# Performance work log

Measured on AMD Instinct MI355X. Metric: run time of the kernel, lower is better.

## Reference

```python
import jax, jax.numpy as jnp
import numpy as np

DIM = 1024
NHEADS = 16
DIM_HEAD = 64
HIDDEN = NHEADS * DIM_HEAD  # 1024


def _xavier(key, fan_in, fan_out):
    limit = np.sqrt(6.0 / (fan_in + fan_out))
    return jax.random.uniform(key, (fan_in, fan_out), jnp.float32, -limit, limit)


def setup_inputs() -> dict:
    key = jax.random.key(0)
    kq, k1, k2, k3 = jax.random.split(key, 4)
    q = jax.random.normal(kq, (2, 2048, DIM), jnp.float32)
    Wq = _xavier(k1, DIM, HIDDEN)
    bq = jnp.zeros((HIDDEN,), jnp.float32)
    Wkv = _xavier(k2, DIM, 2 * HIDDEN)
    bkv = jnp.zeros((2 * HIDDEN,), jnp.float32)
    Wo = _xavier(k3, HIDDEN, DIM)
    bo = jnp.zeros((DIM,), jnp.float32)
    return {"q": q, "Wq": Wq, "bq": bq, "Wkv": Wkv, "bkv": bkv, "Wo": Wo, "bo": bo}


def reference(q, Wq, bq, Wkv, bkv, Wo, bo):
    scale = DIM_HEAD ** (-0.5)
    query = q @ Wq + bq                      # [b, s, hidden]
    kv = q @ Wkv + bkv                       # self-attention: kv from q
    key_, value = jnp.split(kv, 2, axis=-1)  # [b, s, hidden] each
    b, s, _ = query.shape
    query = query.reshape(b, s, NHEADS, DIM_HEAD)
    key_ = key_.reshape(b, s, NHEADS, DIM_HEAD)
    value = value.reshape(b, s, NHEADS, DIM_HEAD)
    scores = jnp.einsum('bqhd,bkhd->bhqk', query, key_) * scale
    attn = jax.nn.softmax(scores, axis=-1)
    out = jnp.einsum('bhqk,bkhd->bqhd', attn, value)
    out = out.reshape(b, s, HIDDEN)
    return out @ Wo + bo
```

## Files before the change

kernel.cpp:

```cpp
#include <hip/hip_runtime.h>

#define DIM 1024
#define NHEADS 16
#define DH 64
#define BATCH 2
#define SEQ 2048

typedef float f32x4 __attribute__((ext_vector_type(4)));
typedef short s16x8 __attribute__((ext_vector_type(8)));
typedef short s16x4 __attribute__((ext_vector_type(4)));

__device__ __forceinline__ short f2bf(float f) {
    union { float f; unsigned u; } v; v.f = f;
    unsigned r = v.u + 0x7fffu + ((v.u >> 16) & 1u);
    return (short)(r >> 16);
}

#if defined(__has_builtin)
#if __has_builtin(__builtin_amdgcn_cvt_pk_bf16_f32)
#define HAVE_PK_BF16 1
#endif
#endif
__device__ __forceinline__ unsigned f2bf_pk(float a, float b) {
#ifdef HAVE_PK_BF16
    typedef __bf16 bf16x2_t __attribute__((ext_vector_type(2)));
    bf16x2_t r = __builtin_amdgcn_cvt_pk_bf16_f32(a, b);
    return __builtin_bit_cast(unsigned, r);
#else
    return ((unsigned)(unsigned short)f2bf(b) << 16) | (unsigned short)f2bf(a);
#endif
}
__device__ __forceinline__ s16x4 pk4(float a, float b, float c, float d) {
    union { unsigned u[2]; s16x4 v; } x;
    x.u[0] = f2bf_pk(a, b); x.u[1] = f2bf_pk(c, d);
    return x.v;
}

#if defined(__has_builtin)
#if __has_builtin(__builtin_amdgcn_exp2f)
#define EXP2(x) __builtin_amdgcn_exp2f(x)
#endif
#endif
#ifndef EXP2
#define EXP2(x) exp2f(x)
#endif

__device__ __forceinline__ void gld16(const void* g, void* l) {
    __builtin_amdgcn_global_load_lds(
        (const __attribute__((address_space(1))) void*)g,
        (__attribute__((address_space(3))) void*)l, 16, 0, 0);
}

__global__ __launch_bounds__(256) void convert_bf16_kernel(
    const float* __restrict__ X, short* __restrict__ Y)
{
    const int i = (blockIdx.x * 256 + threadIdx.x) * 8;
    float4 a = *(const float4*)(X + i);
    float4 b = *(const float4*)(X + i + 4);
    union { unsigned u[4]; s16x8 v; } o;
    o.u[0] = f2bf_pk(a.x, a.y); o.u[1] = f2bf_pk(a.z, a.w);
    o.u[2] = f2bf_pk(b.x, b.y); o.u[3] = f2bf_pk(b.z, b.w);
    *(s16x8*)(Y + i) = o.v;
}

__global__ __launch_bounds__(256) void transpose_w_kernel(
    const float* __restrict__ Wq, const float* __restrict__ Wkv,
    const float* __restrict__ Wo, short* __restrict__ WT)
{
    const int t  = threadIdx.x;
    const int ng = blockIdx.x * 64 + (t & 63);
    const int k0 = (blockIdx.y * 4 + (t >> 6)) * 8;
    const float* W; int n, N;
    if (ng < 1024)      { W = Wq;  n = ng;        N = 1024; }
    else if (ng < 3072) { W = Wkv; n = ng - 1024; N = 2048; }
    else                { W = Wo;  n = ng - 3072; N = 1024; }
    float v[8];
#pragma unroll
    for (int j = 0; j < 8; ++j) v[j] = W[(size_t)(k0 + j) * N + n];
    union { unsigned u[4]; s16x8 s; } o;
    o.u[0] = f2bf_pk(v[0], v[1]); o.u[1] = f2bf_pk(v[2], v[3]);
    o.u[2] = f2bf_pk(v[4], v[5]); o.u[3] = f2bf_pk(v[6], v[7]);
    *(s16x8*)&WT[(size_t)ng * 1024 + k0] = o.s;
}

__global__ __launch_bounds__(256) void transpose_v_kernel(
    const short* __restrict__ QKV, short* __restrict__ VtG)
{
    const int t = threadIdx.x;
    const int tok0 = blockIdx.x * 64;
    const int h = blockIdx.y, b = blockIdx.z;
    __shared__ short L[64 * 72];
    const short* src = QKV + (size_t)(b * SEQ + tok0) * 3072 + 2048 + h * 64;
#pragma unroll
    for (int p = 0; p < 2; ++p) {
        int r = p * 32 + (t >> 3);
        *(s16x8*)&L[r * 72 + (t & 7) * 8] = *(const s16x8*)(src + (size_t)r * 3072 + (t & 7) * 8);
    }
    __syncthreads();
    short* dst = VtG + (size_t)(b * NHEADS + h) * 64 * SEQ + tok0;
#pragma unroll
    for (int p = 0; p < 2; ++p) {
        int u = p * 256 + t;
        int dv = u >> 3, c = (u & 7) * 8;
        s16x8 o;
#pragma unroll
        for (int j = 0; j < 8; ++j) o[j] = L[(c + j) * 72 + dv];
        *(s16x8*)(dst + (size_t)dv * SEQ + c) = o;
    }
}

template<int TM, bool OUT_BF16>
__global__ __launch_bounds__(256) void gemm_mfma_kernel(
    const short* __restrict__ A, const short* __restrict__ Bt,
    const float* __restrict__ bias0, const float* __restrict__ bias1, int nsplit,
    float s0, float s1, void* __restrict__ C, int M, int N)
{
    const int K = 1024;
    constexpr int NI = (TM == 128) ? 4 : 2;
    __shared__ short As[TM * 32];
    __shared__ short Bs[128 * 32];

    const int t    = threadIdx.x;
    const int wave = t >> 6;
    const int lane = t & 63;
    const int col  = lane & 15;
    const int quad = lane >> 4;
    const int m0 = blockIdx.y * TM;
    const int n0 = blockIdx.x * 128;
    const int wroff = (TM == 128) ? (wave >> 1) * 64 : 0;
    const int wcoff = (TM == 128) ? (wave & 1) * 64 : wave * 32;

    f32x4 acc[4][NI];
#pragma unroll
    for (int mi = 0; mi < 4; ++mi)
#pragma unroll
        for (int ni = 0; ni < NI; ++ni) acc[mi][ni] = (f32x4){0.f, 0.f, 0.f, 0.f};

    constexpr int RPW = TM / 4;
    const int ldrowA = wave * RPW + (lane >> 2);
    const int ldrowB = wave * 32  + (lane >> 2);
    const int ldcol  = (lane & 3) * 8;
    const short* Ag = A  + (size_t)(m0 + ldrowA) * K + ldcol;
    const short* Bg = Bt + (size_t)(n0 + ldrowB) * K + ldcol;
    short* AsW = &As[wave * RPW * 32];
    short* BsW = &Bs[wave * 1024];

    for (int k0 = 0; k0 < K; k0 += 32) {
        __syncthreads();
        gld16(Ag + k0, AsW);
        if (TM == 128) gld16(Ag + 16 * K + k0, AsW + 512);
        gld16(Bg + k0,          BsW);
        gld16(Bg + 16 * K + k0, BsW + 512);
        __syncthreads();

        s16x8 aA[4], bB[NI];
#pragma unroll
        for (int mi = 0; mi < 4; ++mi)
            aA[mi] = *(const s16x8*)&As[(wroff + 16 * mi + col) * 32 + quad * 8];
#pragma unroll
        for (int ni = 0; ni < NI; ++ni)
            bB[ni] = *(const s16x8*)&Bs[(wcoff + 16 * ni + col) * 32 + quad * 8];
#pragma unroll
        for (int mi = 0; mi < 4; ++mi)
#pragma unroll
            for (int ni = 0; ni < NI; ++ni)
                acc[mi][ni] = __builtin_amdgcn_mfma_f32_16x16x32_bf16(aA[mi], bB[ni], acc[mi][ni], 0, 0, 0);
    }

    float bias_v[NI], scale_v[NI];
#pragma unroll
    for (int ni = 0; ni < NI; ++ni) {
        int nb = n0 + wcoff + 16 * ni + col;
        bias_v[ni]  = (nb < nsplit) ? bias0[nb] : bias1[nb - nsplit];
        scale_v[ni] = (nb < nsplit) ? s0 : s1;
    }

#pragma unroll
    for (int mi = 0; mi < 4; ++mi)
#pragma unroll
        for (int ni = 0; ni < NI; ++ni)
#pragma unroll
            for (int r = 0; r < 4; ++r) {
                const int gm = m0 + wroff + 16 * mi + quad * 4 + r;
                const int gn = n0 + wcoff + 16 * ni + col;
                float v = (acc[mi][ni][r] + bias_v[ni]) * scale_v[ni];
                if (OUT_BF16) ((short*)C)[(size_t)gm * N + gn] = f2bf(v);
                else          ((float*)C)[(size_t)gm * N + gn] = v;
            }
}

__global__ __launch_bounds__(512) void attn_v6_kernel(
    const short* __restrict__ QKV,
    const short* __restrict__ VtG,
    short* __restrict__ O)
{
    const int qt = blockIdx.x;
    const int h  = blockIdx.y;
    const int b  = blockIdx.z;
    const int t  = threadIdx.x;
    const int wave = t >> 6;
    const int lane = t & 63;
    const int col  = lane & 15;
    const int quad = lane >> 4;
    const int wq = wave & 3;
    const int kh = wave >> 2;

    __shared__ short Ks[2][64 * 72];
    __shared__ short Vt[2][64 * 72];
    __shared__ short Ps[8][64 * 40];

    const short* Qg = QKV + (size_t)(b * SEQ + qt * 256) * 3072 + h * DH;
    const short* Kg = QKV + (size_t)(b * SEQ) * 3072 + 1024 + h * DH;
    const short* VtRow = VtG + (size_t)(b * NHEADS + h) * 64 * SEQ;

    s16x8 aQ[4][2];
#pragma unroll
    for (int tq = 0; tq < 4; ++tq)
#pragma unroll
        for (int kq = 0; kq < 2; ++kq)
            aQ[tq][kq] = *(const s16x8*)(Qg + (size_t)(wq * 64 + 16 * tq + col) * 3072 + kq * 32 + quad * 8);

    f32x4 oa[4][4];
    float lsum[4] = {0.f, 0.f, 0.f, 0.f};
#pragma unroll
    for (int td = 0; td < 4; ++td)
#pragma unroll
        for (int tq = 0; tq < 4; ++tq) oa[td][tq] = (f32x4){0.f, 0.f, 0.f, 0.f};

    const int srow = t >> 3;
    const int sc8  = (t & 7) * 8;
    const short* KgS  = Kg + (size_t)srow * 3072 + sc8;
    const short* VtgS = VtRow + (size_t)srow * SEQ + sc8;
    s16x8 kx = *(const s16x8*)KgS;
    s16x8 vx = *(const s16x8*)VtgS;

    short* PsW = &Ps[wave][0];

    for (int kt = 0; kt < SEQ / 64; ++kt) {
        const int cur = kt & 1;
        *(s16x8*)&Ks[cur][srow * 72 + sc8] = kx;
        *(s16x8*)&Vt[cur][srow * 72 + sc8] = vx;
        {
            int nt = (kt + 1 < SEQ / 64) ? kt + 1 : kt;
            kx = *(const s16x8*)(KgS + (size_t)nt * 64 * 3072);
            vx = *(const s16x8*)(VtgS + (size_t)nt * 64);
        }
        __syncthreads();

        s16x8 aK[2][2];
#pragma unroll
        for (int tk = 0; tk < 2; ++tk)
#pragma unroll
            for (int kq = 0; kq < 2; ++kq)
                aK[tk][kq] = *(const s16x8*)&Ks[cur][(kh * 32 + 16 * tk + col) * 72 + kq * 32 + quad * 8];
        f32x4 st[2][4];
#pragma unroll
        for (int tk = 0; tk < 2; ++tk)
#pragma unroll
            for (int tq = 0; tq < 4; ++tq) {
                f32x4 a = (f32x4){0.f, 0.f, 0.f, 0.f};
                a = __builtin_amdgcn_mfma_f32_16x16x32_bf16(aK[tk][0], aQ[tq][0], a, 0, 0, 0);
                a = __builtin_amdgcn_mfma_f32_16x16x32_bf16(aK[tk][1], aQ[tq][1], a, 0, 0, 0);
                st[tk][tq] = a;
            }

#pragma unroll
        for (int tk = 0; tk < 2; ++tk)
#pragma unroll
            for (int tq = 0; tq < 4; ++tq) {
                float p0 = EXP2(st[tk][tq][0]);
                float p1 = EXP2(st[tk][tq][1]);
                float p2 = EXP2(st[tk][tq][2]);
                float p3 = EXP2(st[tk][tq][3]);
                lsum[tq] += (p0 + p1) + (p2 + p3);
                *(s16x4*)&PsW[(16 * tq + col) * 40 + 16 * tk + quad * 4] = pk4(p0, p1, p2, p3);
            }
        asm volatile("s_waitcnt lgkmcnt(0)" ::: "memory");

        s16x8 bP[4];
#pragma unroll
        for (int tq = 0; tq < 4; ++tq)
            bP[tq] = *(const s16x8*)&PsW[(16 * tq + col) * 40 + quad * 8];
#pragma unroll
        for (int td = 0; td < 4; ++td) {
            const int dv = 16 * td + col;
            s16x8 aV = *(const s16x8*)&Vt[cur][dv * 72 + kh * 32 + quad * 8];
#pragma unroll
            for (int tq = 0; tq < 4; ++tq)
                oa[td][tq] = __builtin_amdgcn_mfma_f32_16x16x32_bf16(aV, bP[tq], oa[td][tq], 0, 0, 0);
        }
    }

#pragma unroll
    for (int tq = 0; tq < 4; ++tq) {
        lsum[tq] += __shfl_xor(lsum[tq], 16);
        lsum[tq] += __shfl_xor(lsum[tq], 32);
    }

    __syncthreads();
    float* red  = (float*)&Ps[0][0];
    float* redl = red + 8192;
#pragma unroll
    for (int round = 0; round < 2; ++round) {
        if (wave >= 4 && ((wave >> 1) & 1) == round) {
            const int slot = wave & 1;
#pragma unroll
            for (int td = 0; td < 4; ++td)
#pragma unroll
                for (int tq = 0; tq < 4; ++tq)
#pragma unroll
                    for (int r = 0; r < 4; ++r)
                        red[slot * 4096 + (16 * td + quad * 4 + r) * 64 + 16 * tq + col] = oa[td][tq][r];
            if (quad == 0)
#pragma unroll
                for (int tq = 0; tq < 4; ++tq)
                    redl[slot * 64 + 16 * tq + col] = lsum[tq];
        }
        __syncthreads();
        if (wave < 4 && ((wave >> 1) & 1) == round) {
            const int slot = wave & 1;
#pragma unroll
            for (int td = 0; td < 4; ++td)
#pragma unroll
                for (int tq = 0; tq < 4; ++tq)
#pragma unroll
                    for (int r = 0; r < 4; ++r)
                        oa[td][tq][r] += red[slot * 4096 + (16 * td + quad * 4 + r) * 64 + 16 * tq + col];
#pragma unroll
            for (int tq = 0; tq < 4; ++tq)
                lsum[tq] += redl[slot * 64 + 16 * tq + col];
        }
        __syncthreads();
    }

    if (wave < 4) {
        short* Og = O + (size_t)(b * SEQ + qt * 256 + wq * 64) * DIM + h * DH;
        float inv[4];
#pragma unroll
        for (int tq = 0; tq < 4; ++tq) inv[tq] = 1.f / lsum[tq];
#pragma unroll
        for (int td = 0; td < 4; ++td)
#pragma unroll
            for (int tq = 0; tq < 4; ++tq)
                *(s16x4*)(Og + (size_t)(16 * tq + col) * DIM + 16 * td + quad * 4) =
                    pk4(oa[td][tq][0] * inv[tq], oa[td][tq][1] * inv[tq],
                        oa[td][tq][2] * inv[tq], oa[td][tq][3] * inv[tq]);
    }
}

extern "C" void kernel_launch(void* const* d_in, const int* in_sizes, int n_in,
                              void* d_out, int out_size, void* d_ws, size_t ws_size,
                              hipStream_t stream)
{
    const float* q   = (const float*)d_in[0];
    const float* Wq  = (const float*)d_in[1];
    const float* bq  = (const float*)d_in[2];
    const float* Wkv = (const float*)d_in[3];
    const float* bkv = (const float*)d_in[4];
    const float* Wo  = (const float*)d_in[5];
    const float* bo  = (const float*)d_in[6];
    float* out = (float*)d_out;

    const int M = BATCH * SEQ;

    short* qb     = (short*)d_ws;
    short* WT     = qb     + (size_t)M * DIM;
    short* QKVbuf = WT     + (size_t)4096 * DIM;
    short* AObuf  = QKVbuf + (size_t)M * 3 * DIM;
    short* VtG    = (short*)d_out;

    const float QSCALE = 0.18033688011112042f;

    convert_bf16_kernel<<<(M * DIM) / (256 * 8), 256, 0, stream>>>(q, qb);
    transpose_w_kernel<<<dim3(64, 32), 256, 0, stream>>>(Wq, Wkv, Wo, WT);

    gemm_mfma_kernel<128, true><<<dim3(3 * DIM / 128, M / 128), 256, 0, stream>>>(
        qb, WT, bq, bkv, DIM, QSCALE, 1.0f, QKVbuf, M, 3 * DIM);
    transpose_v_kernel<<<dim3(SEQ / 64, NHEADS, BATCH), 256, 0, stream>>>(QKVbuf, VtG);
    attn_v6_kernel<<<dim3(SEQ / 256, NHEADS, BATCH), 512, 0, stream>>>(QKVbuf, VtG, AObuf);
    gemm_mfma_kernel<64, false><<<dim3(DIM / 128, M / 64), 256, 0, stream>>>(
        AObuf, WT + (size_t)3072 * 1024, bo, bo, 1 << 30, 1.0f, 1.0f, out, M, DIM);
}
```

Baseline: 199.7 us.

## Keep P in registers via 16x16x16 MFMA, fuse V transpose into QKV GEMM

The attention kernel now feeds exp'd scores straight from accumulator registers as the B operand of 16x16x16 bf16 MFMAs. This drops the per-wave LDS round trip for P and its waitcnt, and shrinks shared memory, which may raise occupancy. The QKV GEMM epilogue writes the V columns already transposed into VtG, so the separate transpose_v kernel is gone. The convert and weight-transpose kernels are merged into one launch. The cost is twice as many MFMA instructions for PV at half the K depth, plus strided 8-byte stores in the GEMM epilogue.

```diff
diff --git a/kernel.cpp b/kernel.cpp
--- a/kernel.cpp
+++ b/kernel.cpp
@@ -45,67 +45,59 @@
 #define EXP2(x) exp2f(x)
 #endif
 
+#if defined(__has_builtin)
+#if __has_builtin(__builtin_amdgcn_mfma_f32_16x16x16bf16_1k)
+#define MFMA16(a, b, c) __builtin_amdgcn_mfma_f32_16x16x16bf16_1k(a, b, c, 0, 0, 0)
+#elif __has_builtin(__builtin_amdgcn_mfma_f32_16x16x16_bf16)
+#define MFMA16(a, b, c) __builtin_amdgcn_mfma_f32_16x16x16_bf16(a, b, c, 0, 0, 0)
+#endif
+#endif
+#ifndef MFMA16
+__device__ __forceinline__ f32x4 mfma16_asm(s16x4 a, s16x4 b, f32x4 c) {
+    f32x4 d;
+    asm volatile("v_mfma_f32_16x16x16_bf16 %0, %1, %2, %3"
+                 : "=v"(d) : "v"(a), "v"(b), "0"(c));
+    return d;
+}
+#define MFMA16(a, b, c) mfma16_asm(a, b, c)
+#endif
+
 __device__ __forceinline__ void gld16(const void* g, void* l) {
     __builtin_amdgcn_global_load_lds(
         (const __attribute__((address_space(1))) void*)g,
         (__attribute__((address_space(3))) void*)l, 16, 0, 0);
 }
 
-__global__ __launch_bounds__(256) void convert_bf16_kernel(
-    const float* __restrict__ X, short* __restrict__ Y)
-{
-    const int i = (blockIdx.x * 256 + threadIdx.x) * 8;
-    float4 a = *(const float4*)(X + i);
-    float4 b = *(const float4*)(X + i + 4);
-    union { unsigned u[4]; s16x8 v; } o;
-    o.u[0] = f2bf_pk(a.x, a.y); o.u[1] = f2bf_pk(a.z, a.w);
-    o.u[2] = f2bf_pk(b.x, b.y); o.u[3] = f2bf_pk(b.z, b.w);
-    *(s16x8*)(Y + i) = o.v;
-}
-
-__global__ __launch_bounds__(256) void transpose_w_kernel(
+__global__ __launch_bounds__(256) void preproc_kernel(
+    const float* __restrict__ q, short* __restrict__ qb,
     const float* __restrict__ Wq, const float* __restrict__ Wkv,
     const float* __restrict__ Wo, short* __restrict__ WT)
 {
-    const int t  = threadIdx.x;
-    const int ng = blockIdx.x * 64 + (t & 63);
-    const int k0 = (blockIdx.y * 4 + (t >> 6)) * 8;
-    const float* W; int n, N;
-    if (ng < 1024)      { W = Wq;  n = ng;        N = 1024; }
-    else if (ng < 3072) { W = Wkv; n = ng - 1024; N = 2048; }
-    else                { W = Wo;  n = ng - 3072; N = 1024; }
-    float v[8];
-#pragma unroll
-    for (int j = 0; j < 8; ++j) v[j] = W[(size_t)(k0 + j) * N + n];
-    union { unsigned u[4]; s16x8 s; } o;
-    o.u[0] = f2bf_pk(v[0], v[1]); o.u[1] = f2bf_pk(v[2], v[3]);
-    o.u[2] = f2bf_pk(v[4], v[5]); o.u[3] = f2bf_pk(v[6], v[7]);
-    *(s16x8*)&WT[(size_t)ng * 1024 + k0] = o.s;
-}
-
-__global__ __launch_bounds__(256) void transpose_v_kernel(
-    const short* __restrict__ QKV, short* __restrict__ VtG)
-{
+    const int bid = blockIdx.x;
     const int t = threadIdx.x;
-    const int tok0 = blockIdx.x * 64;
-    const int h = blockIdx.y, b = blockIdx.z;
-    __shared__ short L[64 * 72];
-    const short* src = QKV + (size_t)(b * SEQ + tok0) * 3072 + 2048 + h * 64;
-#pragma unroll
-    for (int p = 0; p < 2; ++p) {
-        int r = p * 32 + (t >> 3);
-        *(s16x8*)&L[r * 72 + (t & 7) * 8] = *(const s16x8*)(src + (size_t)r * 3072 + (t & 7) * 8);
-    }
-    __syncthreads();
-    short* dst = VtG + (size_t)(b * NHEADS + h) * 64 * SEQ + tok0;
-#pragma unroll
-    for (int p = 0; p < 2; ++p) {
-        int u = p * 256 + t;
-        int dv = u >> 3, c = (u & 7) * 8;
-        s16x8 o;
-#pragma unroll
-        for (int j = 0; j < 8; ++j) o[j] = L[(c + j) * 72 + dv];
-        *(s16x8*)(dst + (size_t)dv * SEQ + c) = o;
+    if (bid < 2048) {
+        const int i = (bid * 256 + t) * 8;
+        float4 a = *(const float4*)(q + i);
+        float4 b = *(const float4*)(q + i + 4);
+        union { unsigned u[4]; s16x8 v; } o;
+        o.u[0] = f2bf_pk(a.x, a.y); o.u[1] = f2bf_pk(a.z, a.w);
+        o.u[2] = f2bf_pk(b.x, b.y); o.u[3] = f2bf_pk(b.z, b.w);
+        *(s16x8*)(qb + i) = o.v;
+    } else {
+        const int tb = bid - 2048;
+        const int ng = (tb & 63) * 64 + (t & 63);
+        const int k0 = ((tb >> 6) * 4 + (t >> 6)) * 8;
+        const float* W; int n, N;
+        if (ng < 1024)      { W = Wq;  n = ng;        N = 1024; }
+        else if (ng < 3072) { W = Wkv; n = ng - 1024; N = 2048; }
+        else                { W = Wo;  n = ng - 3072; N = 1024; }
+        float v[8];
+#pragma unroll
+        for (int j = 0; j < 8; ++j) v[j] = W[(size_t)(k0 + j) * N + n];
+        union { unsigned u[4]; s16x8 s; } o;
+        o.u[0] = f2bf_pk(v[0], v[1]); o.u[1] = f2bf_pk(v[2], v[3]);
+        o.u[2] = f2bf_pk(v[4], v[5]); o.u[3] = f2bf_pk(v[6], v[7]);
+        *(s16x8*)&WT[(size_t)ng * 1024 + k0] = o.s;
     }
 }
 
@@ -113,7 +105,8 @@
 __global__ __launch_bounds__(256) void gemm_mfma_kernel(
     const short* __restrict__ A, const short* __restrict__ Bt,
     const float* __restrict__ bias0, const float* __restrict__ bias1, int nsplit,
-    float s0, float s1, void* __restrict__ C, int M, int N)
+    float s0, float s1, void* __restrict__ C, short* __restrict__ VtG, int vt_split,
+    int M, int N)
 {
     const int K = 1024;
     constexpr int NI = (TM == 128) ? 4 : 2;
@@ -175,21 +168,39 @@
         scale_v[ni] = (nb < nsplit) ? s0 : s1;
     }
 
-#pragma unroll
-    for (int mi = 0; mi < 4; ++mi)
-#pragma unroll
-        for (int ni = 0; ni < NI; ++ni)
-#pragma unroll
-            for (int r = 0; r < 4; ++r) {
-                const int gm = m0 + wroff + 16 * mi + quad * 4 + r;
+    if (vt_split >= 0 && n0 >= vt_split) {
+#pragma unroll
+        for (int mi = 0; mi < 4; ++mi)
+#pragma unroll
+            for (int ni = 0; ni < NI; ++ni) {
+                const int gm = m0 + wroff + 16 * mi + quad * 4;
                 const int gn = n0 + wcoff + 16 * ni + col;
-                float v = (acc[mi][ni][r] + bias_v[ni]) * scale_v[ni];
-                if (OUT_BF16) ((short*)C)[(size_t)gm * N + gn] = f2bf(v);
-                else          ((float*)C)[(size_t)gm * N + gn] = v;
+                const int hv = (gn - vt_split) >> 6;
+                const int dv = (gn - vt_split) & 63;
+                const int bb = gm >> 11, tok = gm & 2047;
+                f32x4 v;
+#pragma unroll
+                for (int r = 0; r < 4; ++r) v[r] = (acc[mi][ni][r] + bias_v[ni]) * scale_v[ni];
+                *(s16x4*)(VtG + (size_t)((bb * NHEADS + hv) * 64 + dv) * SEQ + tok) =
+                    pk4(v[0], v[1], v[2], v[3]);
             }
-}
-
-__global__ __launch_bounds__(512) void attn_v6_kernel(
+    } else {
+#pragma unroll
+        for (int mi = 0; mi < 4; ++mi)
+#pragma unroll
+            for (int ni = 0; ni < NI; ++ni)
+#pragma unroll
+                for (int r = 0; r < 4; ++r) {
+                    const int gm = m0 + wroff + 16 * mi + quad * 4 + r;
+                    const int gn = n0 + wcoff + 16 * ni + col;
+                    float v = (acc[mi][ni][r] + bias_v[ni]) * scale_v[ni];
+                    if (OUT_BF16) ((short*)C)[(size_t)gm * N + gn] = f2bf(v);
+                    else          ((float*)C)[(size_t)gm * N + gn] = v;
+                }
+    }
+}
+
+__global__ __launch_bounds__(512) void attn_v7_kernel(
     const short* __restrict__ QKV,
     const short* __restrict__ VtG,
     short* __restrict__ O)
@@ -205,9 +216,7 @@
     const int wq = wave & 3;
     const int kh = wave >> 2;
 
-    __shared__ short Ks[2][64 * 72];
-    __shared__ short Vt[2][64 * 72];
-    __shared__ short Ps[8][64 * 40];
+    __shared__ short smem[4 * 64 * 72];
 
     const short* Qg = QKV + (size_t)(b * SEQ + qt * 256) * 3072 + h * DH;
     const short* Kg = QKV + (size_t)(b * SEQ) * 3072 + 1024 + h * DH;
@@ -234,12 +243,11 @@
     s16x8 kx = *(const s16x8*)KgS;
     s16x8 vx = *(const s16x8*)VtgS;
 
-    short* PsW = &Ps[wave][0];
-
     for (int kt = 0; kt < SEQ / 64; ++kt) {
-        const int cur = kt & 1;
-        *(s16x8*)&Ks[cur][srow * 72 + sc8] = kx;
-        *(s16x8*)&Vt[cur][srow * 72 + sc8] = vx;
+        const int curK = (kt & 1) * 4608;
+        const int curV = 9216 + (kt & 1) * 4608;
+        *(s16x8*)&smem[curK + srow * 72 + sc8] = kx;
+        *(s16x8*)&smem[curV + srow * 72 + sc8] = vx;
         {
             int nt = (kt + 1 < SEQ / 64) ? kt + 1 : kt;
             kx = *(const s16x8*)(KgS + (size_t)nt * 64 * 3072);
@@ -252,8 +260,9 @@
         for (int tk = 0; tk < 2; ++tk)
 #pragma unroll
             for (int kq = 0; kq < 2; ++kq)
-                aK[tk][kq] = *(const s16x8*)&Ks[cur][(kh * 32 + 16 * tk + col) * 72 + kq * 32 + quad * 8];
-        f32x4 st[2][4];
+                aK[tk][kq] = *(const s16x8*)&smem[curK + (kh * 32 + 16 * tk + col) * 72 + kq * 32 + quad * 8];
+
+        s16x4 bP[2][4];
 #pragma unroll
         for (int tk = 0; tk < 2; ++tk)
 #pragma unroll
@@ -261,33 +270,24 @@
                 f32x4 a = (f32x4){0.f, 0.f, 0.f, 0.f};
                 a = __builtin_amdgcn_mfma_f32_16x16x32_bf16(aK[tk][0], aQ[tq][0], a, 0, 0, 0);
                 a = __builtin_amdgcn_mfma_f32_16x16x32_bf16(aK[tk][1], aQ[tq][1], a, 0, 0, 0);
-                st[tk][tq] = a;
+                float p0 = EXP2(a[0]);
+                float p1 = EXP2(a[1]);
+                float p2 = EXP2(a[2]);
+                float p3 = EXP2(a[3]);
+                lsum[tq] += (p0 + p1) + (p2 + p3);
+                bP[tk][tq] = pk4(p0, p1, p2, p3);
             }
 
-#pragma unroll
-        for (int tk = 0; tk < 2; ++tk)
-#pragma unroll
-            for (int tq = 0; tq < 4; ++tq) {
-                float p0 = EXP2(st[tk][tq][0]);
-                float p1 = EXP2(st[tk][tq][1]);
-                float p2 = EXP2(st[tk][tq][2]);
-                float p3 = EXP2(st[tk][tq][3]);
-                lsum[tq] += (p0 + p1) + (p2 + p3);
-                *(s16x4*)&PsW[(16 * tq + col) * 40 + 16 * tk + quad * 4] = pk4(p0, p1, p2, p3);
-            }
-        asm volatile("s_waitcnt lgkmcnt(0)" ::: "memory");
-
-        s16x8 bP[4];
-#pragma unroll
-        for (int tq = 0; tq < 4; ++tq)
-            bP[tq] = *(const s16x8*)&PsW[(16 * tq + col) * 40 + quad * 8];
 #pragma unroll
         for (int td = 0; td < 4; ++td) {
             const int dv = 16 * td + col;
-            s16x8 aV = *(const s16x8*)&Vt[cur][dv * 72 + kh * 32 + quad * 8];
-#pragma unroll
-            for (int tq = 0; tq < 4; ++tq)
-                oa[td][tq] = __builtin_amdgcn_mfma_f32_16x16x32_bf16(aV, bP[tq], oa[td][tq], 0, 0, 0);
+#pragma unroll
+            for (int tk = 0; tk < 2; ++tk) {
+                s16x4 aV = *(const s16x4*)&smem[curV + dv * 72 + kh * 32 + 16 * tk + quad * 4];
+#pragma unroll
+                for (int tq = 0; tq < 4; ++tq)
+                    oa[td][tq] = MFMA16(aV, bP[tk][tq], oa[td][tq]);
+            }
         }
     }
 
@@ -298,7 +298,7 @@
     }
 
     __syncthreads();
-    float* red  = (float*)&Ps[0][0];
+    float* red  = (float*)smem;
     float* redl = red + 8192;
 #pragma unroll
     for (int round = 0; round < 2; ++round) {
@@ -371,13 +371,11 @@
 
     const float QSCALE = 0.18033688011112042f;
 
-    convert_bf16_kernel<<<(M * DIM) / (256 * 8), 256, 0, stream>>>(q, qb);
-    transpose_w_kernel<<<dim3(64, 32), 256, 0, stream>>>(Wq, Wkv, Wo, WT);
+    preproc_kernel<<<4096, 256, 0, stream>>>(q, qb, Wq, Wkv, Wo, WT);
 
     gemm_mfma_kernel<128, true><<<dim3(3 * DIM / 128, M / 128), 256, 0, stream>>>(
-        qb, WT, bq, bkv, DIM, QSCALE, 1.0f, QKVbuf, M, 3 * DIM);
-    transpose_v_kernel<<<dim3(SEQ / 64, NHEADS, BATCH), 256, 0, stream>>>(QKVbuf, VtG);
-    attn_v6_kernel<<<dim3(SEQ / 256, NHEADS, BATCH), 512, 0, stream>>>(QKVbuf, VtG, AObuf);
+        qb, WT, bq, bkv, DIM, QSCALE, 1.0f, QKVbuf, VtG, 2048, M, 3 * DIM);
+    attn_v7_kernel<<<dim3(SEQ / 256, NHEADS, BATCH), 512, 0, stream>>>(QKVbuf, VtG, AObuf);
     gemm_mfma_kernel<64, false><<<dim3(DIM / 128, M / 64), 256, 0, stream>>>(
-        AObuf, WT + (size_t)3072 * 1024, bo, bo, 1 << 30, 1.0f, 1.0f, out, M, DIM);
-}
+        AObuf, WT + (size_t)3072 * 1024, bo, bo, 1 << 30, 1.0f, 1.0f, out, nullptr, -1, M, DIM);
+}
```

New measurement: 210.0 us. 1.05x slower.
